# Optimization experiments

Hardware: AMD Instinct MI355X
Metric: run time of the kernel (lower is better)

Reference implementation:

```python
import jax, jax.numpy as jnp
from jax import lax
import numpy as np

SEQ, BATCH, HID = 1024, 2048, 64

def setup_inputs() -> dict:
    key = jax.random.key(0)
    ks = jax.random.split(key, 9)
    s = 1.0 / np.sqrt(HID)
    return {
        "x": jax.random.normal(ks[0], (SEQ, BATCH), dtype=jnp.float32),
        "W_ih": jax.random.uniform(ks[1], (4 * HID, 1), jnp.float32, -s, s),
        "W_hh": jax.random.uniform(ks[2], (4 * HID, HID), jnp.float32, -s, s),
        "b_ih": jax.random.uniform(ks[3], (4 * HID,), jnp.float32, -s, s),
        "b_hh": jax.random.uniform(ks[4], (4 * HID,), jnp.float32, -s, s),
        "fc1_w": jax.random.uniform(ks[5], (128, HID), jnp.float32, -s, s),
        "fc1_b": jax.random.uniform(ks[6], (128,), jnp.float32, -s, s),
        "fc2_w": jax.random.uniform(ks[7], (5, 128), jnp.float32, -s, s),
        "fc2_b": jax.random.uniform(ks[8], (5,), jnp.float32, -s, s),
    }

def reference(x, W_ih, W_hh, b_ih, b_hh, fc1_w, fc1_b, fc2_w, fc2_b):
    # x: (S, B) -> unsqueeze(2) gives (S, B, 1); input_size == 1 so the input
    # projection is an outer product, precomputed for all timesteps at once.
    # gx: (S, B, 4H), gate order i, f, g, o (PyTorch convention)
    gx = x[:, :, None] * W_ih[:, 0][None, None, :] + b_ih

    B = x.shape[1]
    h0 = jnp.zeros((B, HID), dtype=x.dtype)
    c0 = jnp.zeros((B, HID), dtype=x.dtype)

    def step(carry, g):
        h, c = carry
        gates = g + h @ W_hh.T + b_hh  # (B, 4H)
        i, f, gg, o = jnp.split(gates, 4, axis=-1)
        i = jax.nn.sigmoid(i)
        f = jax.nn.sigmoid(f)
        gg = jnp.tanh(gg)
        o = jax.nn.sigmoid(o)
        c = f * c + i * gg
        h = o * jnp.tanh(c)
        return (h, c), None

    (h_n, c_n), _ = lax.scan(step, (h0, c0), gx)
    # Original uses hidden[1] == cell state c_n for the MLP head (no activation).
    out = (c_n @ fc1_w.T + fc1_b) @ fc2_w.T + fc2_b  # (B, 5)
    return out
```

## Files before the change

### kernel.cpp

```cpp
#include <hip/hip_runtime.h>
#include <hip/hip_bf16.h>

#define S_LEN 1024
#define BATCH 2048
#define HID   64
#define MB    4
#define NBLK  (BATCH / MB)
#define NTHR  (MB * HID)

typedef _Float16 half8 __attribute__((ext_vector_type(8)));
typedef float    f32x4 __attribute__((ext_vector_type(4)));

#define L2E 1.4426950408889634f
#define HSTRIDE 80

__global__ __launch_bounds__(NTHR, 2) void lstm_kernel(
    const float* __restrict__ x,
    const float* __restrict__ W_ih,
    const float* __restrict__ W_hh,
    const float* __restrict__ b_ih,
    const float* __restrict__ b_hh,
    const float* __restrict__ fc1_w,
    const float* __restrict__ fc1_b,
    const float* __restrict__ fc2_w,
    const float* __restrict__ fc2_b,
    float* __restrict__ out)
{
    __shared__ __align__(16) float    xs[S_LEN * MB];
    __shared__ __align__(16) _Float16 h_buf[2][MB * HSTRIDE];
    __shared__ __align__(16) float    head_lds[MB * HID + MB * 128];

    const int tid  = threadIdx.x;
    const int lane = tid & 63;
    const int wave = tid >> 6;
    const int l15  = lane & 15;
    const int quad = lane >> 4;
    const int b0   = blockIdx.x * MB;

    {
        float4* xs4 = (float4*)xs;
        #pragma unroll
        for (int t = 0; t < 4; ++t) {
            const int s = tid + 256 * t;
            xs4[s] = *(const float4*)(x + (size_t)s * BATCH + b0);
        }
    }

    {
        unsigned* hz = (unsigned*)&h_buf[0][0];
        for (int i = tid; i < 2 * MB * HSTRIDE / 2; i += NTHR) hz[i] = 0u;
    }

    half8 wfrag[4][2];
    #pragma unroll
    for (int g = 0; g < 4; ++g) {
        const float s = (g == 2) ? (-2.0f * L2E) : (-L2E);
        const float* wr = W_hh + (g * 64 + 16 * wave + l15) * HID + quad * 8;
        #pragma unroll
        for (int kt = 0; kt < 2; ++kt) {
            half8 f;
            #pragma unroll
            for (int j = 0; j < 8; ++j) f[j] = (_Float16)(wr[kt * 32 + j] * s);
            wfrag[g][kt] = f;
        }
    }

    const int u = 16 * wave + l15;
    float wih_s[4], bias_s[4];
    #pragma unroll
    for (int g = 0; g < 4; ++g) {
        const int n = g * 64 + u;
        const float s = (g == 2) ? (-2.0f * L2E) : (-L2E);
        wih_s[g]  = W_ih[n] * s;
        bias_s[g] = (b_ih[n] + b_hh[n]) * s;
    }

    float c = 0.0f;
    const f32x4 zero4 = {0.f, 0.f, 0.f, 0.f};

    const _Float16* a0p = &h_buf[0][0] + (l15 >> 2) * HSTRIDE + quad * 8;
    const _Float16* a1p = &h_buf[1][0] + (l15 >> 2) * HSTRIDE + quad * 8;
    _Float16* w0p = &h_buf[0][0] + quad * HSTRIDE + u;
    _Float16* w1p = &h_buf[1][0] + quad * HSTRIDE + u;
    const float* xp = xs + quad;

    __syncthreads();

    auto body = [&](int s, const _Float16* ar, _Float16* hw) {
        const float xv = xp[4 * s];

        half8 a0 = *(const half8*)(ar);
        half8 a1 = *(const half8*)(ar + 32);

        f32x4 acc[4];
        #pragma unroll
        for (int g = 0; g < 4; ++g) {
            acc[g] = __builtin_amdgcn_mfma_f32_16x16x32_f16(a0, wfrag[g][0], zero4, 0, 0, 0);
            acc[g] = __builtin_amdgcn_mfma_f32_16x16x32_f16(a1, wfrag[g][1], acc[g], 0, 0, 0);
        }

        const float gi = acc[0][0] + __builtin_fmaf(xv, wih_s[0], bias_s[0]);
        const float gf = acc[1][0] + __builtin_fmaf(xv, wih_s[1], bias_s[1]);
        const float gg = acc[2][0] + __builtin_fmaf(xv, wih_s[2], bias_s[2]);
        const float go = acc[3][0] + __builtin_fmaf(xv, wih_s[3], bias_s[3]);

        const float eA = __builtin_amdgcn_exp2f(gi);
        const float eF = __builtin_amdgcn_exp2f(gf);
        const float eC = __builtin_amdgcn_exp2f(gg);
        const float eO = __builtin_amdgcn_exp2f(go);

        const float f_ = __builtin_amdgcn_rcpf(1.0f + eF);
        const float R1 = __builtin_amdgcn_rcpf((1.0f + eA) * (1.0f + eC));
        const float ig = __builtin_fmaf(-eC, R1, R1);

        c = __builtin_fmaf(f_, c, ig);

        const float eT = __builtin_amdgcn_exp2f((-2.0f * L2E) * c);
        const float R2 = __builtin_amdgcn_rcpf((1.0f + eO) * (1.0f + eT));
        const float h  = __builtin_fmaf(-eT, R2, R2);

        hw[0] = (_Float16)h;
        __syncthreads();
    };

    for (int s = 0; s < S_LEN; s += 2) {
        body(s,     a0p, w1p);
        body(s + 1, a1p, w0p);
    }

    float* c_lds  = head_lds;
    float* h1_lds = head_lds + MB * HID;
    c_lds[quad * HID + u] = c;
    __syncthreads();

    for (int idx = tid; idx < MB * 128; idx += NTHR) {
        const int b = idx >> 7, j = idx & 127;
        const float* wrow = fc1_w + j * HID;
        const float* crow = c_lds + b * HID;
        float acc = fc1_b[j];
        #pragma unroll
        for (int k = 0; k < HID; k += 4)
            acc += crow[k] * wrow[k] + crow[k+1] * wrow[k+1]
                 + crow[k+2] * wrow[k+2] + crow[k+3] * wrow[k+3];
        h1_lds[idx] = acc;
    }
    __syncthreads();

    if (tid < MB * 5) {
        const int b = tid / 5, q = tid % 5;
        const float* wrow = fc2_w + q * 128;
        const float* hrow = h1_lds + b * 128;
        float acc = fc2_b[q];
        #pragma unroll 4
        for (int j = 0; j < 128; ++j) acc += hrow[j] * wrow[j];
        out[(b0 + b) * 5 + q] = acc;
    }
}

extern "C" void kernel_launch(void* const* d_in, const int* in_sizes, int n_in,
                              void* d_out, int out_size, void* d_ws, size_t ws_size,
                              hipStream_t stream) {
    const float* x     = (const float*)d_in[0];
    const float* W_ih  = (const float*)d_in[1];
    const float* W_hh  = (const float*)d_in[2];
    const float* b_ih  = (const float*)d_in[3];
    const float* b_hh  = (const float*)d_in[4];
    const float* fc1_w = (const float*)d_in[5];
    const float* fc1_b = (const float*)d_in[6];
    const float* fc2_w = (const float*)d_in[7];
    const float* fc2_b = (const float*)d_in[8];
    float* out = (float*)d_out;

    lstm_kernel<<<NBLK, NTHR, 0, stream>>>(x, W_ih, W_hh, b_ih, b_hh,
                                           fc1_w, fc1_b, fc2_w, fc2_b, out);
}
```

Before: 329.2 us.

## Process two independent 4-batch groups per block to interleave recurrence chains

Each block now handles 8 batch elements as two independent groups of 4. The MFMA and gate math for both groups are interleaved within each timestep, so one barrier covers two independent dependency chains. This is meant to hide MFMA and transcendental latency and halve the number of blocks. The x input is also stored transposed in LDS so four timesteps can be read with one float4 load. The cost is higher register pressure (launch bounds drop to one block per SIMD target), more LDS per block, and fewer blocks in flight.

```diff
diff --git a/kernel.cpp b/kernel.cpp
--- a/kernel.cpp
+++ b/kernel.cpp
@@ -4,9 +4,10 @@
 #define S_LEN 1024
 #define BATCH 2048
 #define HID   64
-#define MB    4
+#define GB    4
+#define MB    8
 #define NBLK  (BATCH / MB)
-#define NTHR  (MB * HID)
+#define NTHR  256
 
 typedef _Float16 half8 __attribute__((ext_vector_type(8)));
 typedef float    f32x4 __attribute__((ext_vector_type(4)));
@@ -14,7 +15,7 @@
 #define L2E 1.4426950408889634f
 #define HSTRIDE 80
 
-__global__ __launch_bounds__(NTHR, 2) void lstm_kernel(
+__global__ __launch_bounds__(NTHR, 1) void lstm_kernel(
     const float* __restrict__ x,
     const float* __restrict__ W_ih,
     const float* __restrict__ W_hh,
@@ -26,8 +27,8 @@
     const float* __restrict__ fc2_b,
     float* __restrict__ out)
 {
-    __shared__ __align__(16) float    xs[S_LEN * MB];
-    __shared__ __align__(16) _Float16 h_buf[2][MB * HSTRIDE];
+    __shared__ __align__(16) float    xs_t[MB * S_LEN];
+    __shared__ __align__(16) _Float16 h_buf[2][2][GB * HSTRIDE];
     __shared__ __align__(16) float    head_lds[MB * HID + MB * 128];
 
     const int tid  = threadIdx.x;
@@ -37,30 +38,30 @@
     const int quad = lane >> 4;
     const int b0   = blockIdx.x * MB;
 
+    for (int i = tid; i < S_LEN * 2; i += NTHR) {
+        const int s = i >> 1, hh = (i & 1) * 4;
+        const float4 v = *(const float4*)(x + (size_t)s * BATCH + b0 + hh);
+        xs_t[(hh + 0) * S_LEN + s] = v.x;
+        xs_t[(hh + 1) * S_LEN + s] = v.y;
+        xs_t[(hh + 2) * S_LEN + s] = v.z;
+        xs_t[(hh + 3) * S_LEN + s] = v.w;
+    }
+
     {
-        float4* xs4 = (float4*)xs;
-        #pragma unroll
-        for (int t = 0; t < 4; ++t) {
-            const int s = tid + 256 * t;
-            xs4[s] = *(const float4*)(x + (size_t)s * BATCH + b0);
-        }
-    }
-
-    {
-        unsigned* hz = (unsigned*)&h_buf[0][0];
-        for (int i = tid; i < 2 * MB * HSTRIDE / 2; i += NTHR) hz[i] = 0u;
+        unsigned* hz = (unsigned*)&h_buf[0][0][0];
+        for (int i = tid; i < 2 * 2 * GB * HSTRIDE / 2; i += NTHR) hz[i] = 0u;
     }
 
     half8 wfrag[4][2];
     #pragma unroll
     for (int g = 0; g < 4; ++g) {
-        const float s = (g == 2) ? (-2.0f * L2E) : (-L2E);
+        const float sc = (g == 2) ? (-2.0f * L2E) : (-L2E);
         const float* wr = W_hh + (g * 64 + 16 * wave + l15) * HID + quad * 8;
         #pragma unroll
         for (int kt = 0; kt < 2; ++kt) {
             half8 f;
             #pragma unroll
-            for (int j = 0; j < 8; ++j) f[j] = (_Float16)(wr[kt * 32 + j] * s);
+            for (int j = 0; j < 8; ++j) f[j] = (_Float16)(wr[kt * 32 + j] * sc);
             wfrag[g][kt] = f;
         }
     }
@@ -70,67 +71,107 @@
     #pragma unroll
     for (int g = 0; g < 4; ++g) {
         const int n = g * 64 + u;
-        const float s = (g == 2) ? (-2.0f * L2E) : (-L2E);
-        wih_s[g]  = W_ih[n] * s;
-        bias_s[g] = (b_ih[n] + b_hh[n]) * s;
-    }
-
-    float c = 0.0f;
+        const float sc = (g == 2) ? (-2.0f * L2E) : (-L2E);
+        wih_s[g]  = W_ih[n] * sc;
+        bias_s[g] = (b_ih[n] + b_hh[n]) * sc;
+    }
+
+    float c0 = 0.0f, c1 = 0.0f;
     const f32x4 zero4 = {0.f, 0.f, 0.f, 0.f};
 
-    const _Float16* a0p = &h_buf[0][0] + (l15 >> 2) * HSTRIDE + quad * 8;
-    const _Float16* a1p = &h_buf[1][0] + (l15 >> 2) * HSTRIDE + quad * 8;
-    _Float16* w0p = &h_buf[0][0] + quad * HSTRIDE + u;
-    _Float16* w1p = &h_buf[1][0] + quad * HSTRIDE + u;
-    const float* xp = xs + quad;
+    const _Float16* ar00 = &h_buf[0][0][0] + (l15 >> 2) * HSTRIDE + quad * 8;
+    const _Float16* ar01 = &h_buf[0][1][0] + (l15 >> 2) * HSTRIDE + quad * 8;
+    const _Float16* ar10 = &h_buf[1][0][0] + (l15 >> 2) * HSTRIDE + quad * 8;
+    const _Float16* ar11 = &h_buf[1][1][0] + (l15 >> 2) * HSTRIDE + quad * 8;
+    _Float16* hw00 = &h_buf[0][0][0] + quad * HSTRIDE + u;
+    _Float16* hw01 = &h_buf[0][1][0] + quad * HSTRIDE + u;
+    _Float16* hw10 = &h_buf[1][0][0] + quad * HSTRIDE + u;
+    _Float16* hw11 = &h_buf[1][1][0] + quad * HSTRIDE + u;
+    const float* xg0 = xs_t + quad * S_LEN;
+    const float* xg1 = xs_t + (4 + quad) * S_LEN;
 
     __syncthreads();
 
-    auto body = [&](int s, const _Float16* ar, _Float16* hw) {
-        const float xv = xp[4 * s];
-
-        half8 a0 = *(const half8*)(ar);
-        half8 a1 = *(const half8*)(ar + 32);
-
-        f32x4 acc[4];
+    auto body = [&](const _Float16* ar0, const _Float16* ar1,
+                    _Float16* hw0, _Float16* hw1,
+                    float xv0, float xv1) {
+        half8 a00 = *(const half8*)(ar0);
+        half8 a01 = *(const half8*)(ar0 + 32);
+        half8 a10 = *(const half8*)(ar1);
+        half8 a11 = *(const half8*)(ar1 + 32);
+
+        f32x4 acc0[4], acc1[4];
         #pragma unroll
         for (int g = 0; g < 4; ++g) {
-            acc[g] = __builtin_amdgcn_mfma_f32_16x16x32_f16(a0, wfrag[g][0], zero4, 0, 0, 0);
-            acc[g] = __builtin_amdgcn_mfma_f32_16x16x32_f16(a1, wfrag[g][1], acc[g], 0, 0, 0);
-        }
-
-        const float gi = acc[0][0] + __builtin_fmaf(xv, wih_s[0], bias_s[0]);
-        const float gf = acc[1][0] + __builtin_fmaf(xv, wih_s[1], bias_s[1]);
-        const float gg = acc[2][0] + __builtin_fmaf(xv, wih_s[2], bias_s[2]);
-        const float go = acc[3][0] + __builtin_fmaf(xv, wih_s[3], bias_s[3]);
-
-        const float eA = __builtin_amdgcn_exp2f(gi);
-        const float eF = __builtin_amdgcn_exp2f(gf);
-        const float eC = __builtin_amdgcn_exp2f(gg);
-        const float eO = __builtin_amdgcn_exp2f(go);
-
-        const float f_ = __builtin_amdgcn_rcpf(1.0f + eF);
-        const float R1 = __builtin_amdgcn_rcpf((1.0f + eA) * (1.0f + eC));
-        const float ig = __builtin_fmaf(-eC, R1, R1);
-
-        c = __builtin_fmaf(f_, c, ig);
-
-        const float eT = __builtin_amdgcn_exp2f((-2.0f * L2E) * c);
-        const float R2 = __builtin_amdgcn_rcpf((1.0f + eO) * (1.0f + eT));
-        const float h  = __builtin_fmaf(-eT, R2, R2);
-
-        hw[0] = (_Float16)h;
+            acc0[g] = __builtin_amdgcn_mfma_f32_16x16x32_f16(a00, wfrag[g][0], zero4, 0, 0, 0);
+            acc0[g] = __builtin_amdgcn_mfma_f32_16x16x32_f16(a01, wfrag[g][1], acc0[g], 0, 0, 0);
+        }
+        #pragma unroll
+        for (int g = 0; g < 4; ++g) {
+            acc1[g] = __builtin_amdgcn_mfma_f32_16x16x32_f16(a10, wfrag[g][0], zero4, 0, 0, 0);
+            acc1[g] = __builtin_amdgcn_mfma_f32_16x16x32_f16(a11, wfrag[g][1], acc1[g], 0, 0, 0);
+        }
+
+        {
+            const float gi = acc0[0][0] + __builtin_fmaf(xv0, wih_s[0], bias_s[0]);
+            const float gf = acc0[1][0] + __builtin_fmaf(xv0, wih_s[1], bias_s[1]);
+            const float gg = acc0[2][0] + __builtin_fmaf(xv0, wih_s[2], bias_s[2]);
+            const float go = acc0[3][0] + __builtin_fmaf(xv0, wih_s[3], bias_s[3]);
+
+            const float eA = __builtin_amdgcn_exp2f(gi);
+            const float eF = __builtin_amdgcn_exp2f(gf);
+            const float eC = __builtin_amdgcn_exp2f(gg);
+            const float eO = __builtin_amdgcn_exp2f(go);
+
+            const float f_ = __builtin_amdgcn_rcpf(1.0f + eF);
+            const float R1 = __builtin_amdgcn_rcpf((1.0f + eA) * (1.0f + eC));
+            const float ig = __builtin_fmaf(-eC, R1, R1);
+
+            c0 = __builtin_fmaf(f_, c0, ig);
+
+            const float eT = __builtin_amdgcn_exp2f((-2.0f * L2E) * c0);
+            const float R2 = __builtin_amdgcn_rcpf((1.0f + eO) * (1.0f + eT));
+            const float h  = __builtin_fmaf(-eT, R2, R2);
+            hw0[0] = (_Float16)h;
+        }
+        {
+            const float gi = acc1[0][0] + __builtin_fmaf(xv1, wih_s[0], bias_s[0]);
+            const float gf = acc1[1][0] + __builtin_fmaf(xv1, wih_s[1], bias_s[1]);
+            const float gg = acc1[2][0] + __builtin_fmaf(xv1, wih_s[2], bias_s[2]);
+            const float go = acc1[3][0] + __builtin_fmaf(xv1, wih_s[3], bias_s[3]);
+
+            const float eA = __builtin_amdgcn_exp2f(gi);
+            const float eF = __builtin_amdgcn_exp2f(gf);
+            const float eC = __builtin_amdgcn_exp2f(gg);
+            const float eO = __builtin_amdgcn_exp2f(go);
+
+            const float f_ = __builtin_amdgcn_rcpf(1.0f + eF);
+            const float R1 = __builtin_amdgcn_rcpf((1.0f + eA) * (1.0f + eC));
+            const float ig = __builtin_fmaf(-eC, R1, R1);
+
+            c1 = __builtin_fmaf(f_, c1, ig);
+
+            const float eT = __builtin_amdgcn_exp2f((-2.0f * L2E) * c1);
+            const float R2 = __builtin_amdgcn_rcpf((1.0f + eO) * (1.0f + eT));
+            const float h  = __builtin_fmaf(-eT, R2, R2);
+            hw1[0] = (_Float16)h;
+        }
         __syncthreads();
     };
 
-    for (int s = 0; s < S_LEN; s += 2) {
-        body(s,     a0p, w1p);
-        body(s + 1, a1p, w0p);
+    for (int s = 0; s < S_LEN; s += 4) {
+        const float4 x0 = *(const float4*)(xg0 + s);
+        const float4 x1 = *(const float4*)(xg1 + s);
+        body(ar00, ar10, hw01, hw11, x0.x, x1.x);
+        body(ar01, ar11, hw00, hw10, x0.y, x1.y);
+        body(ar00, ar10, hw01, hw11, x0.z, x1.z);
+        body(ar01, ar11, hw00, hw10, x0.w, x1.w);
     }
 
     float* c_lds  = head_lds;
     float* h1_lds = head_lds + MB * HID;
-    c_lds[quad * HID + u] = c;
+    c_lds[quad * HID + u]       = c0;
+    c_lds[(4 + quad) * HID + u] = c1;
     __syncthreads();
 
     for (int idx = tid; idx < MB * 128; idx += NTHR) {
```

New measurement: 427.4 us. 29.8% more time.

## Assign one batch row per wave to remove per-step block barriers

Applied to the files above, without the earlier changes.

The recurrent work is remapped so each wave owns a single batch row and computes all 64 hidden units. The wave therefore holds all four column tiles of W_hh per gate. Because the hidden state a wave reads each step is produced only by that same wave, the per-timestep __syncthreads and the double-buffered h array are removed in favour of a single LDS row per batch element. The cost is four times more MFMA work and weight registers per wave, since most rows of each 16x16 tile are redundant and only one output element is selected per lane.

```diff
diff --git a/kernel.cpp b/kernel.cpp
--- a/kernel.cpp
+++ b/kernel.cpp
@@ -6,13 +6,12 @@
 #define HID   64
 #define MB    4
 #define NBLK  (BATCH / MB)
-#define NTHR  (MB * HID)
+#define NTHR  256
 
 typedef _Float16 half8 __attribute__((ext_vector_type(8)));
 typedef float    f32x4 __attribute__((ext_vector_type(4)));
 
 #define L2E 1.4426950408889634f
-#define HSTRIDE 80
 
 __global__ __launch_bounds__(NTHR, 2) void lstm_kernel(
     const float* __restrict__ x,
@@ -27,12 +26,12 @@
     float* __restrict__ out)
 {
     __shared__ __align__(16) float    xs[S_LEN * MB];
-    __shared__ __align__(16) _Float16 h_buf[2][MB * HSTRIDE];
+    __shared__ __align__(16) _Float16 h_lds[MB][HID];
     __shared__ __align__(16) float    head_lds[MB * HID + MB * 128];
 
     const int tid  = threadIdx.x;
     const int lane = tid & 63;
-    const int wave = tid >> 6;
+    const int wr   = tid >> 6;
     const int l15  = lane & 15;
     const int quad = lane >> 4;
     const int b0   = blockIdx.x * MB;
@@ -46,68 +45,78 @@
         }
     }
 
-    {
-        unsigned* hz = (unsigned*)&h_buf[0][0];
-        for (int i = tid; i < 2 * MB * HSTRIDE / 2; i += NTHR) hz[i] = 0u;
-    }
+    if (tid < MB * HID / 2) ((unsigned*)h_lds)[tid] = 0u;
 
-    half8 wfrag[4][2];
+    half8 wfrag[4][4][2];
     #pragma unroll
     for (int g = 0; g < 4; ++g) {
-        const float s = (g == 2) ? (-2.0f * L2E) : (-L2E);
-        const float* wr = W_hh + (g * 64 + 16 * wave + l15) * HID + quad * 8;
+        const float sc = (g == 2) ? (-2.0f * L2E) : (-L2E);
         #pragma unroll
-        for (int kt = 0; kt < 2; ++kt) {
-            half8 f;
+        for (int ct = 0; ct < 4; ++ct) {
+            const float* wrow = W_hh + (g * 64 + ct * 16 + l15) * HID + quad * 8;
             #pragma unroll
-            for (int j = 0; j < 8; ++j) f[j] = (_Float16)(wr[kt * 32 + j] * s);
-            wfrag[g][kt] = f;
+            for (int kt = 0; kt < 2; ++kt) {
+                const float4 v0 = *(const float4*)(wrow + kt * 32);
+                const float4 v1 = *(const float4*)(wrow + kt * 32 + 4);
+                half8 f;
+                f[0] = (_Float16)(v0.x * sc); f[1] = (_Float16)(v0.y * sc);
+                f[2] = (_Float16)(v0.z * sc); f[3] = (_Float16)(v0.w * sc);
+                f[4] = (_Float16)(v1.x * sc); f[5] = (_Float16)(v1.y * sc);
+                f[6] = (_Float16)(v1.z * sc); f[7] = (_Float16)(v1.w * sc);
+                wfrag[g][ct][kt] = f;
+            }
         }
     }
 
-    const int u = 16 * wave + l15;
+    const int u = lane;
     float wih_s[4], bias_s[4];
     #pragma unroll
     for (int g = 0; g < 4; ++g) {
         const int n = g * 64 + u;
-        const float s = (g == 2) ? (-2.0f * L2E) : (-L2E);
-        wih_s[g]  = W_ih[n] * s;
-        bias_s[g] = (b_ih[n] + b_hh[n]) * s;
+        const float sc = (g == 2) ? (-2.0f * L2E) : (-L2E);
+        wih_s[g]  = W_ih[n] * sc;
+        bias_s[g] = (b_ih[n] + b_hh[n]) * sc;
     }
 
     float c = 0.0f;
     const f32x4 zero4 = {0.f, 0.f, 0.f, 0.f};
 
-    const _Float16* a0p = &h_buf[0][0] + (l15 >> 2) * HSTRIDE + quad * 8;
-    const _Float16* a1p = &h_buf[1][0] + (l15 >> 2) * HSTRIDE + quad * 8;
-    _Float16* w0p = &h_buf[0][0] + quad * HSTRIDE + u;
-    _Float16* w1p = &h_buf[1][0] + quad * HSTRIDE + u;
-    const float* xp = xs + quad;
+    const _Float16* arp = &h_lds[wr][0] + quad * 8;
+    _Float16*       hwp = &h_lds[wr][0] + lane;
+    const float*    xp  = xs + wr;
+
+    const bool q0  = (quad == 0);
+    const bool q2  = (quad == 2);
+    const bool qlo = (quad < 2);
 
     __syncthreads();
 
-    auto body = [&](int s, const _Float16* ar, _Float16* hw) {
+    #pragma unroll 1
+    for (int s = 0; s < S_LEN; ++s) {
+        half8 a0 = *(const half8*)(arp);
+        half8 a1 = *(const half8*)(arp + 32);
         const float xv = xp[4 * s];
 
-        half8 a0 = *(const half8*)(ar);
-        half8 a1 = *(const half8*)(ar + 32);
-
-        f32x4 acc[4];
+        float gate[4];
         #pragma unroll
         for (int g = 0; g < 4; ++g) {
-            acc[g] = __builtin_amdgcn_mfma_f32_16x16x32_f16(a0, wfrag[g][0], zero4, 0, 0, 0);
-            acc[g] = __builtin_amdgcn_mfma_f32_16x16x32_f16(a1, wfrag[g][1], acc[g], 0, 0, 0);
+            f32x4 acc0 = __builtin_amdgcn_mfma_f32_16x16x32_f16(a0, wfrag[g][0][0], zero4, 0, 0, 0);
+            f32x4 acc1 = __builtin_amdgcn_mfma_f32_16x16x32_f16(a0, wfrag[g][1][0], zero4, 0, 0, 0);
+            f32x4 acc2 = __builtin_amdgcn_mfma_f32_16x16x32_f16(a0, wfrag[g][2][0], zero4, 0, 0, 0);
+            f32x4 acc3 = __builtin_amdgcn_mfma_f32_16x16x32_f16(a0, wfrag[g][3][0], zero4, 0, 0, 0);
+            acc0 = __builtin_amdgcn_mfma_f32_16x16x32_f16(a1, wfrag[g][0][1], acc0, 0, 0, 0);
+            acc1 = __builtin_amdgcn_mfma_f32_16x16x32_f16(a1, wfrag[g][1][1], acc1, 0, 0, 0);
+            acc2 = __builtin_amdgcn_mfma_f32_16x16x32_f16(a1, wfrag[g][2][1], acc2, 0, 0, 0);
+            acc3 = __builtin_amdgcn_mfma_f32_16x16x32_f16(a1, wfrag[g][3][1], acc3, 0, 0, 0);
+            const float v01 = q0 ? acc0[0] : acc1[0];
+            const float v23 = q2 ? acc2[0] : acc3[0];
+            gate[g] = (qlo ? v01 : v23) + __builtin_fmaf(xv, wih_s[g], bias_s[g]);
         }
 
-        const float gi = acc[0][0] + __builtin_fmaf(xv, wih_s[0], bias_s[0]);
-        const float gf = acc[1][0] + __builtin_fmaf(xv, wih_s[1], bias_s[1]);
-        const float gg = acc[2][0] + __builtin_fmaf(xv, wih_s[2], bias_s[2]);
-        const float go = acc[3][0] + __builtin_fmaf(xv, wih_s[3], bias_s[3]);
-
-        const float eA = __builtin_amdgcn_exp2f(gi);
-        const float eF = __builtin_amdgcn_exp2f(gf);
-        const float eC = __builtin_amdgcn_exp2f(gg);
-        const float eO = __builtin_amdgcn_exp2f(go);
+        const float eA = __builtin_amdgcn_exp2f(gate[0]);
+        const float eF = __builtin_amdgcn_exp2f(gate[1]);
+        const float eC = __builtin_amdgcn_exp2f(gate[2]);
+        const float eO = __builtin_amdgcn_exp2f(gate[3]);
 
         const float f_ = __builtin_amdgcn_rcpf(1.0f + eF);
         const float R1 = __builtin_amdgcn_rcpf((1.0f + eA) * (1.0f + eC));
@@ -119,18 +128,12 @@
         const float R2 = __builtin_amdgcn_rcpf((1.0f + eO) * (1.0f + eT));
         const float h  = __builtin_fmaf(-eT, R2, R2);
 
-        hw[0] = (_Float16)h;
-        __syncthreads();
-    };
-
-    for (int s = 0; s < S_LEN; s += 2) {
-        body(s,     a0p, w1p);
-        body(s + 1, a1p, w0p);
+        hwp[0] = (_Float16)h;
     }
 
     float* c_lds  = head_lds;
     float* h1_lds = head_lds + MB * HID;
-    c_lds[quad * HID + u] = c;
+    c_lds[wr * HID + u] = c;
     __syncthreads();
 
     for (int idx = tid; idx < MB * 128; idx += NTHR) {
```

New measurement: 736.8 us. 2.24x slower.

## Ping-pong two independent batch groups per block to overlap MFMA and elementwise

Applied to the files above, without the earlier changes.

Each block now handles 8 batch rows split into two independent groups of 4 waves. In each half-step one group runs the recurrent MFMA while the other runs the gate nonlinearities, so the two phases of the serial recurrence interleave across groups. Each group keeps a single h buffer, with two barriers per step separating reads and writes. The gate math also merges two reciprocals into one via a shared product. This halves the block count and doubles the barriers per step, and the shared reciprocal slightly changes rounding.

```diff
diff --git a/kernel.cpp b/kernel.cpp
--- a/kernel.cpp
+++ b/kernel.cpp
@@ -4,9 +4,9 @@
 #define S_LEN 1024
 #define BATCH 2048
 #define HID   64
-#define MB    4
+#define MB    8
 #define NBLK  (BATCH / MB)
-#define NTHR  (MB * HID)
+#define NTHR  512
 
 typedef _Float16 half8 __attribute__((ext_vector_type(8)));
 typedef float    f32x4 __attribute__((ext_vector_type(4)));
@@ -27,7 +27,7 @@
     float* __restrict__ out)
 {
     __shared__ __align__(16) float    xs[S_LEN * MB];
-    __shared__ __align__(16) _Float16 h_buf[2][MB * HSTRIDE];
+    __shared__ __align__(16) _Float16 h_lds[2][4 * HSTRIDE];
     __shared__ __align__(16) float    head_lds[MB * HID + MB * 128];
 
     const int tid  = threadIdx.x;
@@ -37,68 +37,70 @@
     const int quad = lane >> 4;
     const int b0   = blockIdx.x * MB;
 
+    const bool gA  = (wave < 4);
+    const int  wg  = wave & 3;
+    const int  rowl = (gA ? quad : 4 + quad);
+
     {
         float4* xs4 = (float4*)xs;
         #pragma unroll
         for (int t = 0; t < 4; ++t) {
-            const int s = tid + 256 * t;
-            xs4[s] = *(const float4*)(x + (size_t)s * BATCH + b0);
+            const int idx = tid + 512 * t;
+            const int s = idx >> 1, hh = (idx & 1) * 4;
+            xs4[idx] = *(const float4*)(x + (size_t)s * BATCH + b0 + hh);
         }
     }
 
-    {
-        unsigned* hz = (unsigned*)&h_buf[0][0];
-        for (int i = tid; i < 2 * MB * HSTRIDE / 2; i += NTHR) hz[i] = 0u;
-    }
+    if (tid < 320) ((unsigned*)h_lds)[tid] = 0u;
 
     half8 wfrag[4][2];
     #pragma unroll
     for (int g = 0; g < 4; ++g) {
-        const float s = (g == 2) ? (-2.0f * L2E) : (-L2E);
-        const float* wr = W_hh + (g * 64 + 16 * wave + l15) * HID + quad * 8;
+        const float sc = (g == 2) ? (-2.0f * L2E) : (-L2E);
+        const float* wr = W_hh + (g * 64 + 16 * wg + l15) * HID + quad * 8;
         #pragma unroll
         for (int kt = 0; kt < 2; ++kt) {
             half8 f;
             #pragma unroll
-            for (int j = 0; j < 8; ++j) f[j] = (_Float16)(wr[kt * 32 + j] * s);
+            for (int j = 0; j < 8; ++j) f[j] = (_Float16)(wr[kt * 32 + j] * sc);
             wfrag[g][kt] = f;
         }
     }
 
-    const int u = 16 * wave + l15;
+    const int u = 16 * wg + l15;
     float wih_s[4], bias_s[4];
     #pragma unroll
     for (int g = 0; g < 4; ++g) {
         const int n = g * 64 + u;
-        const float s = (g == 2) ? (-2.0f * L2E) : (-L2E);
-        wih_s[g]  = W_ih[n] * s;
-        bias_s[g] = (b_ih[n] + b_hh[n]) * s;
+        const float sc = (g == 2) ? (-2.0f * L2E) : (-L2E);
+        wih_s[g]  = W_ih[n] * sc;
+        bias_s[g] = (b_ih[n] + b_hh[n]) * sc;
     }
 
     float c = 0.0f;
     const f32x4 zero4 = {0.f, 0.f, 0.f, 0.f};
 
-    const _Float16* a0p = &h_buf[0][0] + (l15 >> 2) * HSTRIDE + quad * 8;
-    const _Float16* a1p = &h_buf[1][0] + (l15 >> 2) * HSTRIDE + quad * 8;
-    _Float16* w0p = &h_buf[0][0] + quad * HSTRIDE + u;
-    _Float16* w1p = &h_buf[1][0] + quad * HSTRIDE + u;
-    const float* xp = xs + quad;
+    _Float16* hbase = &h_lds[gA ? 0 : 1][0];
+    const _Float16* arp = hbase + (l15 >> 2) * HSTRIDE + quad * 8;
+    _Float16*       hwp = hbase + quad * HSTRIDE + u;
+    const float*    xp  = xs + rowl;
 
-    __syncthreads();
+    f32x4 acc[4];
+    #pragma unroll
+    for (int g = 0; g < 4; ++g) acc[g] = zero4;
 
-    auto body = [&](int s, const _Float16* ar, _Float16* hw) {
-        const float xv = xp[4 * s];
-
-        half8 a0 = *(const half8*)(ar);
-        half8 a1 = *(const half8*)(ar + 32);
-
-        f32x4 acc[4];
+    auto do_mfma = [&]() {
+        half8 a0 = *(const half8*)(arp);
+        half8 a1 = *(const half8*)(arp + 32);
         #pragma unroll
         for (int g = 0; g < 4; ++g) {
             acc[g] = __builtin_amdgcn_mfma_f32_16x16x32_f16(a0, wfrag[g][0], zero4, 0, 0, 0);
             acc[g] = __builtin_amdgcn_mfma_f32_16x16x32_f16(a1, wfrag[g][1], acc[g], 0, 0, 0);
         }
+    };
 
+    auto do_ew = [&](int s) {
+        const float xv = xp[8 * s];
         const float gi = acc[0][0] + __builtin_fmaf(xv, wih_s[0], bias_s[0]);
         const float gf = acc[1][0] + __builtin_fmaf(xv, wih_s[1], bias_s[1]);
         const float gg = acc[2][0] + __builtin_fmaf(xv, wih_s[2], bias_s[2]);
@@ -109,8 +111,11 @@
         const float eC = __builtin_amdgcn_exp2f(gg);
         const float eO = __builtin_amdgcn_exp2f(go);
 
-        const float f_ = __builtin_amdgcn_rcpf(1.0f + eF);
-        const float R1 = __builtin_amdgcn_rcpf((1.0f + eA) * (1.0f + eC));
+        const float P  = 1.0f + eF;
+        const float Q  = (1.0f + eA) * (1.0f + eC);
+        const float r  = __builtin_amdgcn_rcpf(P * Q);
+        const float f_ = r * Q;
+        const float R1 = r * P;
         const float ig = __builtin_fmaf(-eC, R1, R1);
 
         c = __builtin_fmaf(f_, c, ig);
@@ -119,30 +124,34 @@
         const float R2 = __builtin_amdgcn_rcpf((1.0f + eO) * (1.0f + eT));
         const float h  = __builtin_fmaf(-eT, R2, R2);
 
-        hw[0] = (_Float16)h;
-        __syncthreads();
+        hwp[0] = (_Float16)h;
     };
 
-    for (int s = 0; s < S_LEN; s += 2) {
-        body(s,     a0p, w1p);
-        body(s + 1, a1p, w0p);
+    __syncthreads();
+
+    #pragma unroll 1
+    for (int s = 0; s < S_LEN; ++s) {
+        if (gA) do_ew(s); else do_mfma();
+        __syncthreads();
+        if (gA) { if (s + 1 < S_LEN) do_mfma(); } else do_ew(s);
+        __syncthreads();
     }
 
     float* c_lds  = head_lds;
     float* h1_lds = head_lds + MB * HID;
-    c_lds[quad * HID + u] = c;
+    c_lds[rowl * HID + u] = c;
     __syncthreads();
 
     for (int idx = tid; idx < MB * 128; idx += NTHR) {
         const int b = idx >> 7, j = idx & 127;
         const float* wrow = fc1_w + j * HID;
         const float* crow = c_lds + b * HID;
-        float acc = fc1_b[j];
+        float acc2 = fc1_b[j];
         #pragma unroll
         for (int k = 0; k < HID; k += 4)
-            acc += crow[k] * wrow[k] + crow[k+1] * wrow[k+1]
-                 + crow[k+2] * wrow[k+2] + crow[k+3] * wrow[k+3];
-        h1_lds[idx] = acc;
+            acc2 += crow[k] * wrow[k] + crow[k+1] * wrow[k+1]
+                  + crow[k+2] * wrow[k+2] + crow[k+3] * wrow[k+3];
+        h1_lds[idx] = acc2;
     }
     __syncthreads();
 
@@ -150,10 +159,10 @@
         const int b = tid / 5, q = tid % 5;
         const float* wrow = fc2_w + q * 128;
         const float* hrow = h1_lds + b * 128;
-        float acc = fc2_b[q];
+        float acc2 = fc2_b[q];
         #pragma unroll 4
-        for (int j = 0; j < 128; ++j) acc += hrow[j] * wrow[j];
-        out[(b0 + b) * 5 + q] = acc;
+        for (int j = 0; j < 128; ++j) acc2 += hrow[j] * wrow[j];
+        out[(b0 + b) * 5 + q] = acc2;
     }
 }
 
```

Result: slower. 517.6 us (+57.3%).
